# Kernel tuning notes

Measured on AMD Instinct MI355X. Metric: run time of the kernel, lower is better.

Reference implementation:

```python
import jax, jax.numpy as jnp
import numpy as np

D_MODEL = 512
N_HEADS = 8
MAX_CH = 128
LN_EPS = 1e-5


def setup_inputs() -> dict:
    key = jax.random.key(0)
    ks = jax.random.split(key, 8)
    B, T, C, D = 8, 256, 64, D_MODEL
    x = jax.random.normal(ks[0], (B, T, C, D), dtype=jnp.float32)
    # nn.MultiheadAttention params: packed in_proj [3D, D], out_proj [D, D]
    in_proj_w = jax.random.normal(ks[1], (3 * D, D), dtype=jnp.float32) * 0.02
    in_proj_b = jnp.zeros((3 * D,), dtype=jnp.float32)
    out_proj_w = jax.random.normal(ks[2], (D, D), dtype=jnp.float32) * 0.02
    out_proj_b = jnp.zeros((D,), dtype=jnp.float32)
    ln_g = jnp.ones((D,), dtype=jnp.float32)
    ln_b = jnp.zeros((D,), dtype=jnp.float32)
    rel_pos_bias = jax.random.normal(ks[3], (N_HEADS, MAX_CH, MAX_CH), dtype=jnp.float32) * 0.02
    return {"x": x, "in_proj_w": in_proj_w, "in_proj_b": in_proj_b,
            "out_proj_w": out_proj_w, "out_proj_b": out_proj_b,
            "ln_g": ln_g, "ln_b": ln_b, "rel_pos_bias": rel_pos_bias}


def _layernorm(x, g, b):
    mu = jnp.mean(x, axis=-1, keepdims=True)
    var = jnp.var(x, axis=-1, keepdims=True)
    return (x - mu) * jax.lax.rsqrt(var + LN_EPS) * g + b


def reference(x, in_proj_w, in_proj_b, out_proj_w, out_proj_b, ln_g, ln_b, rel_pos_bias):
    B, T, C, D = x.shape
    H = N_HEADS
    hd = D // H
    N = B * T
    xf = x.reshape(N, C, D)
    # 2D additive attn_mask: mean over heads of rel-pos bias, broadcast over heads/batch
    bias = jnp.mean(rel_pos_bias[:, :C, :C], axis=0)  # [C, C]
    qkv = xf @ in_proj_w.T + in_proj_b  # [N, C, 3D]
    q, k, v = jnp.split(qkv, 3, axis=-1)
    q = q.reshape(N, C, H, hd)
    k = k.reshape(N, C, H, hd)
    v = v.reshape(N, C, H, hd)
    scores = jnp.einsum('nqhd,nkhd->nhqk', q, k) / jnp.sqrt(jnp.float32(hd))
    scores = scores + bias[None, None, :, :]
    attn = jax.nn.softmax(scores, axis=-1)
    ctx = jnp.einsum('nhqk,nkhd->nqhd', attn, v).reshape(N, C, D)
    attn_out = ctx @ out_proj_w.T + out_proj_b
    out = _layernorm(xf + attn_out, ln_g, ln_b)
    return out.reshape(B, T, C, D)
```

## Files before the change

### kernel.cpp

```cpp
#include <hip/hip_runtime.h>
#include <stdint.h>
#include <stddef.h>


typedef __attribute__((ext_vector_type(8))) short short8;
typedef __attribute__((ext_vector_type(4))) float f32x4;

typedef __attribute__((address_space(3))) unsigned int as3_u32;
typedef __attribute__((address_space(1))) unsigned int as1_u32;

#define VMCNT8 asm volatile("s_waitcnt vmcnt(8)" ::: "memory")
#define VMCNT5 asm volatile("s_waitcnt vmcnt(5)" ::: "memory")
#define VMCNT4 asm volatile("s_waitcnt vmcnt(4)" ::: "memory")
#define VMCNT0 asm volatile("s_waitcnt vmcnt(0)" ::: "memory")
#define LGKM0  asm volatile("s_waitcnt lgkmcnt(0)" ::: "memory")
#define BARR() __builtin_amdgcn_s_barrier()
#define PRIO1  __builtin_amdgcn_s_setprio(1)
#define PRIO0  __builtin_amdgcn_s_setprio(0)

__device__ __forceinline__ unsigned short f2bf(float f) {
  unsigned u = __builtin_bit_cast(unsigned, f);
  u = (u + 0x7FFFu + ((u >> 16) & 1u)) >> 16;
  return (unsigned short)u;
}

__device__ __forceinline__ f32x4 mfma16(short8 a, short8 b, f32x4 c) {
  return __builtin_amdgcn_mfma_f32_16x16x32_bf16(a, b, c, 0, 0, 0);
}

__device__ __forceinline__ short8 rd8s(const char* buf, int row, int unit) {
  return *(const short8*)(buf + row * 128 + ((unit ^ (row & 7)) * 16));
}
__device__ __forceinline__ void wr2s(char* buf, int row, int col, unsigned short v) {
  int slot = (col >> 3) ^ (row & 7);
  *(unsigned short*)(buf + row * 128 + slot * 16 + (col & 7) * 2) = v;
}
__device__ __forceinline__ void wr8s(char* buf, int row, int col, uint2 v) {
  int slot = (col >> 3) ^ (row & 7);
  *(uint2*)(buf + row * 128 + slot * 16 + (col & 7) * 2) = v;
}

__device__ __forceinline__ void stage16k(char* ldsbase, const char* gsrc, int w, int lane) {
#pragma unroll
  for (int j = 0; j < 4; ++j) {
    int off = j * 4096 + w * 1024;
    __builtin_amdgcn_global_load_lds((const as1_u32*)(gsrc + off + lane * 16),
                                     (as3_u32*)(ldsbase + off), 16, 0, 0);
  }
}

__global__ void prep_kernel(const float* __restrict__ x,
                            const float* __restrict__ wqkv_f,
                            const float* __restrict__ wo_f,
                            const float* __restrict__ rel,
                            unsigned short* __restrict__ wt,
                            float* __restrict__ bias2d,
                            char* __restrict__ dout) {
  int b = blockIdx.x, tid = threadIdx.x;
  if (b < 8192) {
    int n = b >> 2, kc = b & 3;
    unsigned short* dst =
        (unsigned short*)(dout + (size_t)n * 131072 + 65536 + kc * 16384);
    const float* src0 = x + (size_t)n * 32768 + kc * 128;
#pragma unroll
    for (int t = 0; t < 4; ++t) {
      int u = t * 256 + tid;
      int row = u >> 4, us = u & 15;
      int kg = (us & 8) | ((us ^ row) & 7);
      const float* src = src0 + row * 512 + kg * 8;
      float4 a = *(const float4*)src;
      float4 c = *(const float4*)(src + 4);
      unsigned p0 = (unsigned)f2bf(a.x) | ((unsigned)f2bf(a.y) << 16);
      unsigned p1 = (unsigned)f2bf(a.z) | ((unsigned)f2bf(a.w) << 16);
      unsigned p2 = (unsigned)f2bf(c.x) | ((unsigned)f2bf(c.y) << 16);
      unsigned p3 = (unsigned)f2bf(c.z) | ((unsigned)f2bf(c.w) << 16);
      *(uint4*)(dst + u * 8) = make_uint4(p0, p1, p2, p3);
    }
  } else if (b < 8320) {
    int cb = b - 8192;
    unsigned short* dst = wt + (size_t)cb * 8192;
#pragma unroll
    for (int t = 0; t < 4; ++t) {
      int u = t * 256 + tid;
      int row = u >> 4, us = u & 15;
      int kg = (us & 8) | ((us ^ row) & 7);
      const float* src;
      if (cb < 96) {
        int h = cb / 12, j = cb % 12;
        int kc = j / 3, rg = j % 3;
        src = wqkv_f + (size_t)(rg * 512 + h * 64 + row) * 512 + kc * 128 + kg * 8;
      } else {
        int cw = cb - 96;
        int kc = cw >> 3, ng = cw & 7;
        src = wo_f + (size_t)(ng * 64 + row) * 512 + kc * 128 + kg * 8;
      }
      float4 a = *(const float4*)src;
      float4 c = *(const float4*)(src + 4);
      unsigned p0 = (unsigned)f2bf(a.x) | ((unsigned)f2bf(a.y) << 16);
      unsigned p1 = (unsigned)f2bf(a.z) | ((unsigned)f2bf(a.w) << 16);
      unsigned p2 = (unsigned)f2bf(c.x) | ((unsigned)f2bf(c.y) << 16);
      unsigned p3 = (unsigned)f2bf(c.z) | ((unsigned)f2bf(c.w) << 16);
      *(uint4*)(dst + u * 8) = make_uint4(p0, p1, p2, p3);
    }
  } else {
    int idx = (b - 8320) * 256 + tid;
    int m = idx >> 6, nn = idx & 63;
    float s = 0.f;
#pragma unroll
    for (int hh = 0; hh < 8; ++hh) s += rel[hh * 16384 + m * 128 + nn];
    bias2d[idx] = s * 0.125f;
  }
}

__global__ __launch_bounds__(256, 2) void attn_qkv(
    const char* __restrict__ wq,
    const float* __restrict__ bqkv,
    const float* __restrict__ bias2d,
    char* __restrict__ ctxg) {
  extern __shared__ __attribute__((aligned(16))) char smem[];
  char* WSw = smem;
  char* WSx = smem + 32768;
  char* B0 = smem + 49152;
  char* B1 = smem + 57344;
  char* B2 = smem + 65536;
  float* BQ = (float*)(smem + 73728);

  const int n = blockIdx.x;
  const int tid = threadIdx.x;
  const int w = tid >> 6, lane = tid & 63;
  const int l15 = lane & 15, g = lane >> 4;
  const int wm = w >> 1, wn = w & 1;
  const int mrow = w * 16 + g * 4;
  const int wrow = w * 16 + l15;

  const char* xsrc = ctxg + (size_t)n * 131072 + 65536;

#pragma unroll
  for (int i = 0; i < 6; ++i) BQ[i * 256 + tid] = bqkv[i * 256 + tid];
  float b2d[16];
#pragma unroll
  for (int nt = 0; nt < 4; ++nt)
#pragma unroll
    for (int r = 0; r < 4; ++r)
      b2d[nt * 4 + r] = bias2d[(mrow + r) * 64 + nt * 16 + l15];
  VMCNT0; LGKM0; BARR();

  stage16k(WSx, xsrc, w, lane);
  stage16k(WSw, wq, w, lane);

  for (int h = 0; h < 8; ++h) {
    f32x4 aq[2][2] = {}, ak[2][2] = {}, av[2][2] = {};
    const bool lh = (h == 7);
#pragma unroll
    for (int kc = 0; kc < 4; ++kc) {
      const int i = h * 12 + kc * 3;
      const bool lt = lh && (kc == 3);
      stage16k(WSw + ((i + 1) & 1) * 16384, wq + (size_t)(i + 1) * 16384, w, lane);
      VMCNT4; BARR();
      short8 xq[8];
#pragma unroll
      for (int mt = 0; mt < 2; ++mt)
#pragma unroll
        for (int ks = 0; ks < 4; ++ks) {
          int row = wm * 32 + mt * 16 + l15;
          int u = ks * 4 + g;
          int us = (u & 8) | ((u ^ row) & 7);
          xq[mt * 4 + ks] = *(const short8*)(WSx + row * 256 + us * 16);
        }
      {
        const char* ws = WSw + (i & 1) * 16384;
        PRIO1;
#pragma unroll
        for (int ks = 0; ks < 4; ++ks)
#pragma unroll
          for (int nt = 0; nt < 2; ++nt) {
            int row = wn * 32 + nt * 16 + l15;
            int kg = ks * 4 + g;
            int us = (kg & 8) | ((kg ^ row) & 7);
            short8 bfr = *(const short8*)(ws + row * 256 + us * 16);
            aq[0][nt] = mfma16(xq[ks], bfr, aq[0][nt]);
            aq[1][nt] = mfma16(xq[4 + ks], bfr, aq[1][nt]);
          }
        PRIO0;
      }
      BARR();
      stage16k(WSw + ((i + 2) & 1) * 16384, wq + (size_t)(i + 2) * 16384, w, lane);
      if (!lt) stage16k(WSx, xsrc + (size_t)((kc + 1) & 3) * 16384, w, lane);
      if (lt) { VMCNT4; } else { VMCNT8; }
      BARR();
      {
        const char* ws = WSw + ((i + 1) & 1) * 16384;
        PRIO1;
#pragma unroll
        for (int ks = 0; ks < 4; ++ks)
#pragma unroll
          for (int nt = 0; nt < 2; ++nt) {
            int row = wn * 32 + nt * 16 + l15;
            int kg = ks * 4 + g;
            int us = (kg & 8) | ((kg ^ row) & 7);
            short8 bfr = *(const short8*)(ws + row * 256 + us * 16);
            ak[0][nt] = mfma16(xq[ks], bfr, ak[0][nt]);
            ak[1][nt] = mfma16(xq[4 + ks], bfr, ak[1][nt]);
          }
        PRIO0;
      }
      BARR();
      if (i + 3 < 96)
        stage16k(WSw + ((i + 3) & 1) * 16384, wq + (size_t)(i + 3) * 16384, w, lane);
      if (lt) { VMCNT0; } else { VMCNT8; }
      BARR();
      {
        const char* ws = WSw + ((i + 2) & 1) * 16384;
        PRIO1;
#pragma unroll
        for (int ks = 0; ks < 4; ++ks)
#pragma unroll
          for (int nt = 0; nt < 2; ++nt) {
            int row = wn * 32 + nt * 16 + l15;
            int kg = ks * 4 + g;
            int us = (kg & 8) | ((kg ^ row) & 7);
            short8 bfr = *(const short8*)(ws + row * 256 + us * 16);
            av[0][nt] = mfma16(xq[ks], bfr, av[0][nt]);
            av[1][nt] = mfma16(xq[4 + ks], bfr, av[1][nt]);
          }
        PRIO0;
      }
      BARR();
    }

    {
      float bq2[2], bk2[2], bv2[2];
#pragma unroll
      for (int nt = 0; nt < 2; ++nt) {
        int col = h * 64 + wn * 32 + nt * 16 + l15;
        bq2[nt] = BQ[col];
        bk2[nt] = BQ[512 + col];
        bv2[nt] = BQ[1024 + col];
      }
#pragma unroll
      for (int mt = 0; mt < 2; ++mt)
#pragma unroll
        for (int nt = 0; nt < 2; ++nt) {
          int rowb = wm * 32 + mt * 16 + g * 4;
          int col = wn * 32 + nt * 16 + l15;
#pragma unroll
          for (int r = 0; r < 4; ++r) {
            wr2s(B0, rowb + r, col, f2bf(aq[mt][nt][r] + bq2[nt]));
            wr2s(B1, rowb + r, col, f2bf(ak[mt][nt][r] + bk2[nt]));
          }
          unsigned short p0 = f2bf(av[mt][nt][0] + bv2[nt]);
          unsigned short p1 = f2bf(av[mt][nt][1] + bv2[nt]);
          unsigned short p2 = f2bf(av[mt][nt][2] + bv2[nt]);
          unsigned short p3 = f2bf(av[mt][nt][3] + bv2[nt]);
          unsigned lo = (unsigned)p0 | ((unsigned)p1 << 16);
          unsigned hi = (unsigned)p2 | ((unsigned)p3 << 16);
          wr8s(B2, col, rowb, make_uint2(lo, hi));
        }
    }
    LGKM0; BARR();

    {
      f32x4 sc[4] = {};
      short8 aq0 = rd8s(B0, wrow, g);
      short8 aq1 = rd8s(B0, wrow, 4 + g);
#pragma unroll
      for (int nt = 0; nt < 4; ++nt)
        sc[nt] = mfma16(aq0, rd8s(B1, nt * 16 + l15, g), sc[nt]);
#pragma unroll
      for (int nt = 0; nt < 4; ++nt)
        sc[nt] = mfma16(aq1, rd8s(B1, nt * 16 + l15, 4 + g), sc[nt]);
      float mx[4] = {-1e30f, -1e30f, -1e30f, -1e30f};
#pragma unroll
      for (int nt = 0; nt < 4; ++nt)
#pragma unroll
        for (int r = 0; r < 4; ++r) {
          float v = sc[nt][r] * 0.125f + b2d[nt * 4 + r];
          sc[nt][r] = v;
          mx[r] = fmaxf(mx[r], v);
        }
#pragma unroll
      for (int mk = 1; mk < 16; mk <<= 1)
#pragma unroll
        for (int r = 0; r < 4; ++r) mx[r] = fmaxf(mx[r], __shfl_xor(mx[r], mk));
      float sm[4] = {0.f, 0.f, 0.f, 0.f};
#pragma unroll
      for (int nt = 0; nt < 4; ++nt)
#pragma unroll
        for (int r = 0; r < 4; ++r) {
          float e = __expf(sc[nt][r] - mx[r]);
          sc[nt][r] = e;
          sm[r] += e;
        }
#pragma unroll
      for (int mk = 1; mk < 16; mk <<= 1)
#pragma unroll
        for (int r = 0; r < 4; ++r) sm[r] += __shfl_xor(sm[r], mk);
      float inv[4];
#pragma unroll
      for (int r = 0; r < 4; ++r) inv[r] = 1.0f / sm[r];
#pragma unroll
      for (int nt = 0; nt < 4; ++nt)
#pragma unroll
        for (int r = 0; r < 4; ++r)
          wr2s(B0, mrow + r, nt * 16 + l15, f2bf(sc[nt][r] * inv[r]));
    }

    f32x4 cv[4] = {};
    {
      short8 ap0 = rd8s(B0, wrow, g);
      short8 ap1 = rd8s(B0, wrow, 4 + g);
#pragma unroll
      for (int nt = 0; nt < 4; ++nt)
        cv[nt] = mfma16(ap0, rd8s(B2, nt * 16 + l15, g), cv[nt]);
#pragma unroll
      for (int nt = 0; nt < 4; ++nt)
        cv[nt] = mfma16(ap1, rd8s(B2, nt * 16 + l15, 4 + g), cv[nt]);
    }
    BARR();
#pragma unroll
    for (int nt = 0; nt < 4; ++nt)
#pragma unroll
      for (int r = 0; r < 4; ++r)
        wr2s(B1, mrow + r, nt * 16 + l15, f2bf(cv[nt][r]));
    LGKM0; BARR();

    {
      char* cdst = ctxg + (size_t)n * 131072 + h * 8192;
#pragma unroll
      for (int it = 0; it < 2; ++it) {
        int flat = it * 256 + tid;
        int row = flat >> 3, s = flat & 7;
        uint4 v = *(const uint4*)(B1 + row * 128 + s * 16);
        *(uint4*)(cdst + row * 128 + s * 16) = v;
      }
    }
  }
}

__global__ __launch_bounds__(256, 2) void oproj_ln(
    const char* __restrict__ ctxg,
    const char* __restrict__ wo,
    const float* __restrict__ bo,
    const float* __restrict__ x,
    const float* __restrict__ lng,
    const float* __restrict__ lnb,
    float* __restrict__ out) {
  __shared__ __attribute__((aligned(16))) char smem[65536];
  char* WB = smem;
  char* CB = smem + 32768;
  float* EP  = (float*)smem;
  float* SM1 = (float*)(smem + 32768);
  float* SM2 = (float*)(smem + 33408);

  const int n = blockIdx.x;
  const int tid = threadIdx.x;
  const int w = tid >> 6, lane = tid & 63;
  const int l15 = lane & 15, g = lane >> 4;
  const int um = w >> 1, un = w & 1;

  const char* cbase = ctxg + (size_t)n * 131072;

  stage16k(CB, cbase, w, lane);
  stage16k(WB, wo, w, lane);

  f32x4 acc[8][2][2] = {};

  for (int kc = 0; kc < 4; ++kc) {
    short8 actx[2][4];
#pragma unroll
    for (int ng = 0; ng < 8; ++ng) {
      int b = kc * 8 + ng;
      if (b < 31)
        stage16k(WB + (((b + 1) & 1) << 14), wo + (size_t)(b + 1) * 16384, w, lane);
      if ((ng & 1) == 0 && kc < 3) {
        int p = ng >> 1;
        int off = p * 4096 + w * 1024;
        __builtin_amdgcn_global_load_lds(
            (const as1_u32*)(cbase + (kc + 1) * 16384 + off + lane * 16),
            (as3_u32*)(CB + (((kc + 1) & 1) << 14) + off), 16, 0, 0);
      }
      if (b < 31) { VMCNT5; } else { VMCNT0; }
      BARR();
      const char* cb = CB + ((kc & 1) << 14);
      if (ng == 0) {
#pragma unroll
        for (int mt = 0; mt < 2; ++mt)
#pragma unroll
          for (int ks = 0; ks < 4; ++ks) {
            int row = um * 32 + mt * 16 + l15;
            int u = ks * 4 + g;
            actx[mt][ks] = *(const short8*)(cb + (u >> 3) * 8192 + row * 128 +
                                            (((u & 7) ^ (row & 7)) * 16));
          }
      }
      const char* ws = WB + ((b & 1) << 14);
      PRIO1;
#pragma unroll
      for (int ks = 0; ks < 4; ++ks) {
#pragma unroll
        for (int nt = 0; nt < 2; ++nt) {
          int row = un * 32 + nt * 16 + l15;
          int kg = ks * 4 + g;
          int us = (kg & 8) | ((kg ^ row) & 7);
          short8 bfr = *(const short8*)(ws + row * 256 + us * 16);
          acc[ng][0][nt] = mfma16(actx[0][ks], bfr, acc[ng][0][nt]);
          acc[ng][1][nt] = mfma16(actx[1][ks], bfr, acc[ng][1][nt]);
        }
      }
      PRIO0;
      BARR();
    }
  }

  VMCNT0;
  const float* xblk = x + (size_t)n * 32768;
  float* oblk = out + (size_t)n * 32768;
  float s1[2][4] = {}, s2[2][4] = {};

#pragma unroll
  for (int ng = 0; ng < 8; ++ng) {
#pragma unroll
    for (int t = 0; t < 4; ++t) {
      int flat = t * 256 + tid;
      int row = flat >> 4, f4 = flat & 15;
      float4 v = *(const float4*)(xblk + row * 512 + ng * 64 + f4 * 4);
      *(float4*)(EP + row * 68 + f4 * 4) = v;
    }
    LGKM0; BARR();
    float boA[2];
#pragma unroll
    for (int nt = 0; nt < 2; ++nt) boA[nt] = bo[ng * 64 + un * 32 + nt * 16 + l15];
#pragma unroll
    for (int mt = 0; mt < 2; ++mt)
#pragma unroll
      for (int nt = 0; nt < 2; ++nt)
#pragma unroll
        for (int r = 0; r < 4; ++r) {
          int row = um * 32 + mt * 16 + g * 4 + r;
          float xv = EP[row * 68 + un * 32 + nt * 16 + l15];
          float v = acc[ng][mt][nt][r] + boA[nt] + xv;
          acc[ng][mt][nt][r] = v;
          s1[mt][r] += v;
          s2[mt][r] += v * v;
        }
    LGKM0; BARR();
  }
#pragma unroll
  for (int mk = 1; mk < 16; mk <<= 1)
#pragma unroll
    for (int mt = 0; mt < 2; ++mt)
#pragma unroll
      for (int r = 0; r < 4; ++r) {
        s1[mt][r] += __shfl_xor(s1[mt][r], mk);
        s2[mt][r] += __shfl_xor(s2[mt][r], mk);
      }
  if (l15 == 0) {
#pragma unroll
    for (int mt = 0; mt < 2; ++mt)
#pragma unroll
      for (int r = 0; r < 4; ++r) {
        int row = um * 32 + mt * 16 + g * 4 + r;
        SM1[row * 2 + un] = s1[mt][r];
        SM2[row * 2 + un] = s2[mt][r];
      }
  }
  LGKM0; BARR();
  float mu[2][4], rs[2][4];
#pragma unroll
  for (int mt = 0; mt < 2; ++mt)
#pragma unroll
    for (int r = 0; r < 4; ++r) {
      int row = um * 32 + mt * 16 + g * 4 + r;
      float a1 = SM1[row * 2] + SM1[row * 2 + 1];
      float a2 = SM2[row * 2] + SM2[row * 2 + 1];
      float m = a1 * (1.0f / 512.0f);
      float var = a2 * (1.0f / 512.0f) - m * m;
      mu[mt][r] = m;
      rs[mt][r] = rsqrtf(var + 1e-5f);
    }
  BARR();
#pragma unroll
  for (int ng = 0; ng < 8; ++ng) {
    float lgA[2], lbA[2];
#pragma unroll
    for (int nt = 0; nt < 2; ++nt) {
      int col = ng * 64 + un * 32 + nt * 16 + l15;
      lgA[nt] = lng[col];
      lbA[nt] = lnb[col];
    }
#pragma unroll
    for (int mt = 0; mt < 2; ++mt)
#pragma unroll
      for (int nt = 0; nt < 2; ++nt)
#pragma unroll
        for (int r = 0; r < 4; ++r) {
          int row = um * 32 + mt * 16 + g * 4 + r;
          EP[row * 68 + un * 32 + nt * 16 + l15] =
              (acc[ng][mt][nt][r] - mu[mt][r]) * rs[mt][r] * lgA[nt] + lbA[nt];
        }
    LGKM0; BARR();
#pragma unroll
    for (int t = 0; t < 4; ++t) {
      int flat = t * 256 + tid;
      int row = flat >> 4, f4 = flat & 15;
      *(float4*)(oblk + row * 512 + ng * 64 + f4 * 4) =
          *(const float4*)(EP + row * 68 + f4 * 4);
    }
    BARR();
  }
}

extern "C" void kernel_launch(void* const* d_in, const int* in_sizes, int n_in,
                              void* d_out, int out_size, void* d_ws, size_t ws_size,
                              hipStream_t stream) {
  const float* x    = (const float*)d_in[0];
  const float* wqkv = (const float*)d_in[1];
  const float* bqkv = (const float*)d_in[2];
  const float* wo   = (const float*)d_in[3];
  const float* bo   = (const float*)d_in[4];
  const float* lng  = (const float*)d_in[5];
  const float* lnb  = (const float*)d_in[6];
  const float* rel  = (const float*)d_in[7];

  unsigned short* wt = (unsigned short*)d_ws;
  float* bias2d = (float*)((char*)d_ws + 128 * 16384);
  const char* wqc = (const char*)d_ws;
  const char* woc = (const char*)d_ws + 96 * 16384;

  hipFuncSetAttribute(reinterpret_cast<const void*>(attn_qkv),
                      hipFuncAttributeMaxDynamicSharedMemorySize, 79872);

  prep_kernel<<<8336, 256, 0, stream>>>(x, wqkv, wo, rel, wt, bias2d,
                                        (char*)d_out);
  attn_qkv<<<2048, 256, 79872, stream>>>(wqc, bqkv, bias2d, (char*)d_out);
  oproj_ln<<<2048, 256, 0, stream>>>((const char*)d_out, woc, bo, x, lng, lnb,
                                     (float*)d_out);
}
```

Measured before the change: 573.8 us.

## Load x fragments directly to registers and triple-buffer weight tiles in LDS

The prep kernel now writes the bf16 x tile in a k-unit-major layout, so each lane can load its MFMA A-fragments straight from global memory into registers. This drops the LDS staging of x. The QKV projection loop now uses three LDS weight buffers (one each for Q, K and V) with deeper vmcnt waits, which removes one barrier phase per k-chunk and lets more weight loads stay in flight. In exchange, x fragments are re-read from global or L2 memory for every head instead of from LDS, and the direct global loads add latency on the critical path.

```diff
diff --git a/kernel.cpp b/kernel.cpp
--- a/kernel.cpp
+++ b/kernel.cpp
@@ -9,6 +9,7 @@
 typedef __attribute__((address_space(3))) unsigned int as3_u32;
 typedef __attribute__((address_space(1))) unsigned int as1_u32;
 
+#define VMCNT12 asm volatile("s_waitcnt vmcnt(12)" ::: "memory")
 #define VMCNT8 asm volatile("s_waitcnt vmcnt(8)" ::: "memory")
 #define VMCNT5 asm volatile("s_waitcnt vmcnt(5)" ::: "memory")
 #define VMCNT4 asm volatile("s_waitcnt vmcnt(4)" ::: "memory")
@@ -47,6 +48,35 @@
     __builtin_amdgcn_global_load_lds((const as1_u32*)(gsrc + off + lane * 16),
                                      (as3_u32*)(ldsbase + off), 16, 0, 0);
   }
+}
+
+__device__ __forceinline__ void load_xq(short8* xq, const char* xqbase,
+                                        int wm, int l15, int g) {
+#pragma unroll
+  for (int mt = 0; mt < 2; ++mt)
+#pragma unroll
+    for (int ks = 0; ks < 4; ++ks) {
+      int row = wm * 32 + mt * 16 + l15;
+      int u = ks * 4 + g;
+      xq[mt * 4 + ks] = *(const short8*)(xqbase + u * 1024 + row * 16);
+    }
+}
+
+__device__ __forceinline__ void proj_body(const char* ws, const short8* xq,
+                                          int wn, int l15, int g, f32x4 acc[2][2]) {
+  PRIO1;
+#pragma unroll
+  for (int ks = 0; ks < 4; ++ks)
+#pragma unroll
+    for (int nt = 0; nt < 2; ++nt) {
+      int row = wn * 32 + nt * 16 + l15;
+      int kg = ks * 4 + g;
+      int us = (kg & 8) | ((kg ^ row) & 7);
+      short8 bfr = *(const short8*)(ws + row * 256 + us * 16);
+      acc[0][nt] = mfma16(xq[ks], bfr, acc[0][nt]);
+      acc[1][nt] = mfma16(xq[4 + ks], bfr, acc[1][nt]);
+    }
+  PRIO0;
 }
 
 __global__ void prep_kernel(const float* __restrict__ x,
@@ -64,17 +94,16 @@
     const float* src0 = x + (size_t)n * 32768 + kc * 128;
 #pragma unroll
     for (int t = 0; t < 4; ++t) {
-      int u = t * 256 + tid;
-      int row = u >> 4, us = u & 15;
-      int kg = (us & 8) | ((us ^ row) & 7);
-      const float* src = src0 + row * 512 + kg * 8;
+      int row = t * 16 + (tid >> 4);
+      int u = tid & 15;
+      const float* src = src0 + row * 512 + u * 8;
       float4 a = *(const float4*)src;
       float4 c = *(const float4*)(src + 4);
       unsigned p0 = (unsigned)f2bf(a.x) | ((unsigned)f2bf(a.y) << 16);
       unsigned p1 = (unsigned)f2bf(a.z) | ((unsigned)f2bf(a.w) << 16);
       unsigned p2 = (unsigned)f2bf(c.x) | ((unsigned)f2bf(c.y) << 16);
       unsigned p3 = (unsigned)f2bf(c.z) | ((unsigned)f2bf(c.w) << 16);
-      *(uint4*)(dst + u * 8) = make_uint4(p0, p1, p2, p3);
+      *(uint4*)(dst + (u * 64 + row) * 8) = make_uint4(p0, p1, p2, p3);
     }
   } else if (b < 8320) {
     int cb = b - 8192;
@@ -118,8 +147,7 @@
     const float* __restrict__ bias2d,
     char* __restrict__ ctxg) {
   extern __shared__ __attribute__((aligned(16))) char smem[];
-  char* WSw = smem;
-  char* WSx = smem + 32768;
+  char* WR = smem;
   char* B0 = smem + 49152;
   char* B1 = smem + 57344;
   char* B2 = smem + 65536;
@@ -145,87 +173,32 @@
       b2d[nt * 4 + r] = bias2d[(mrow + r) * 64 + nt * 16 + l15];
   VMCNT0; LGKM0; BARR();
 
-  stage16k(WSx, xsrc, w, lane);
-  stage16k(WSw, wq, w, lane);
+  short8 xq[8];
+  load_xq(xq, xsrc, wm, l15, g);
+  stage16k(WR, wq, w, lane);
 
   for (int h = 0; h < 8; ++h) {
     f32x4 aq[2][2] = {}, ak[2][2] = {}, av[2][2] = {};
-    const bool lh = (h == 7);
 #pragma unroll
     for (int kc = 0; kc < 4; ++kc) {
-      const int i = h * 12 + kc * 3;
-      const bool lt = lh && (kc == 3);
-      stage16k(WSw + ((i + 1) & 1) * 16384, wq + (size_t)(i + 1) * 16384, w, lane);
+      const int j = h * 12 + kc * 3;
+      stage16k(WR + 16384, wq + (size_t)(j + 1) * 16384, w, lane);
+      if (h == 0 && kc == 0) { VMCNT4; } else { VMCNT12; }
+      BARR();
+      proj_body(WR, xq, wn, l15, g, aq);
+      stage16k(WR + 32768, wq + (size_t)(j + 2) * 16384, w, lane);
       VMCNT4; BARR();
-      short8 xq[8];
-#pragma unroll
-      for (int mt = 0; mt < 2; ++mt)
-#pragma unroll
-        for (int ks = 0; ks < 4; ++ks) {
-          int row = wm * 32 + mt * 16 + l15;
-          int u = ks * 4 + g;
-          int us = (u & 8) | ((u ^ row) & 7);
-          xq[mt * 4 + ks] = *(const short8*)(WSx + row * 256 + us * 16);
-        }
-      {
-        const char* ws = WSw + (i & 1) * 16384;
-        PRIO1;
-#pragma unroll
-        for (int ks = 0; ks < 4; ++ks)
-#pragma unroll
-          for (int nt = 0; nt < 2; ++nt) {
-            int row = wn * 32 + nt * 16 + l15;
-            int kg = ks * 4 + g;
-            int us = (kg & 8) | ((kg ^ row) & 7);
-            short8 bfr = *(const short8*)(ws + row * 256 + us * 16);
-            aq[0][nt] = mfma16(xq[ks], bfr, aq[0][nt]);
-            aq[1][nt] = mfma16(xq[4 + ks], bfr, aq[1][nt]);
-          }
-        PRIO0;
+      proj_body(WR + 16384, xq, wn, l15, g, ak);
+      if (j + 3 < 96) {
+        stage16k(WR, wq + (size_t)(j + 3) * 16384, w, lane);
+        VMCNT4;
+      } else {
+        VMCNT0;
       }
       BARR();
-      stage16k(WSw + ((i + 2) & 1) * 16384, wq + (size_t)(i + 2) * 16384, w, lane);
-      if (!lt) stage16k(WSx, xsrc + (size_t)((kc + 1) & 3) * 16384, w, lane);
-      if (lt) { VMCNT4; } else { VMCNT8; }
-      BARR();
-      {
-        const char* ws = WSw + ((i + 1) & 1) * 16384;
-        PRIO1;
-#pragma unroll
-        for (int ks = 0; ks < 4; ++ks)
-#pragma unroll
-          for (int nt = 0; nt < 2; ++nt) {
-            int row = wn * 32 + nt * 16 + l15;
-            int kg = ks * 4 + g;
-            int us = (kg & 8) | ((kg ^ row) & 7);
-            short8 bfr = *(const short8*)(ws + row * 256 + us * 16);
-            ak[0][nt] = mfma16(xq[ks], bfr, ak[0][nt]);
-            ak[1][nt] = mfma16(xq[4 + ks], bfr, ak[1][nt]);
-          }
-        PRIO0;
-      }
-      BARR();
-      if (i + 3 < 96)
-        stage16k(WSw + ((i + 3) & 1) * 16384, wq + (size_t)(i + 3) * 16384, w, lane);
-      if (lt) { VMCNT0; } else { VMCNT8; }
-      BARR();
-      {
-        const char* ws = WSw + ((i + 2) & 1) * 16384;
-        PRIO1;
-#pragma unroll
-        for (int ks = 0; ks < 4; ++ks)
-#pragma unroll
-          for (int nt = 0; nt < 2; ++nt) {
-            int row = wn * 32 + nt * 16 + l15;
-            int kg = ks * 4 + g;
-            int us = (kg & 8) | ((kg ^ row) & 7);
-            short8 bfr = *(const short8*)(ws + row * 256 + us * 16);
-            av[0][nt] = mfma16(xq[ks], bfr, av[0][nt]);
-            av[1][nt] = mfma16(xq[4 + ks], bfr, av[1][nt]);
-          }
-        PRIO0;
-      }
-      BARR();
+      proj_body(WR + 32768, xq, wn, l15, g, av);
+      if (!(h == 7 && kc == 3))
+        load_xq(xq, xsrc + (size_t)((kc + 1) & 3) * 16384, wm, l15, g);
     }
 
     {
```

Result: slower. 589.4 us (+2.7%).
